# Kernel tuning notes

Hardware: AMD Instinct MI355X
Metric: run time of the kernel (lower is better)

## Reference

```python
import jax, jax.numpy as jnp
import numpy as np

N = 50000; R2 = 200; D = 200; E = 200000; B = 1024
NB = 4; NF = 96; KS = 7; KW = 10; KH = 20
FLAT = (2 * KW - KS + 1) * (KH - KS + 1) * NF  # 18816
EPS = 1e-5


def _bn2d(x, g, b):
    # BatchNorm2d over NCHW with batch statistics
    m = x.mean(axis=(0, 2, 3), keepdims=True)
    v = x.var(axis=(0, 2, 3), keepdims=True)
    return (x - m) * jax.lax.rsqrt(v + EPS) * g[None, :, None, None] + b[None, :, None, None]


def _bn1d(x, g, b):
    m = x.mean(axis=0, keepdims=True)
    v = x.var(axis=0, keepdims=True)
    return (x - m) * jax.lax.rsqrt(v + EPS) * g[None, :] + b[None, :]


def setup_inputs() -> dict:
    key = jax.random.key(0)
    ks = jax.random.split(key, 16)
    s = 0.05
    return {
        'ent_emb': jax.random.normal(ks[0], (N, D)) * s,
        'rel_table': jax.random.normal(ks[1], (R2, D)) * s,
        'basis': jax.random.normal(ks[2], (NB, D, D)) * s,
        'att': jax.random.normal(ks[3], (R2, NB)) * s,
        'root': jax.random.normal(ks[4], (D, D)) * s,
        'gbias': jnp.zeros((D,), jnp.float32),
        'bn0_g': jnp.ones((1,), jnp.float32), 'bn0_b': jnp.zeros((1,), jnp.float32),
        'conv_k': jax.random.normal(ks[5], (NF, 1, KS, KS)) * s,
        'conv_b': jnp.zeros((NF,), jnp.float32),
        'bn1_g': jnp.ones((NF,), jnp.float32), 'bn1_b': jnp.zeros((NF,), jnp.float32),
        'fc_W': jax.random.normal(ks[6], (FLAT, D)) * s,
        'fc_b': jnp.zeros((D,), jnp.float32),
        'bn2_g': jnp.ones((D,), jnp.float32), 'bn2_b': jnp.zeros((D,), jnp.float32),
        'ent_bias': jnp.zeros((N,), jnp.float32),
        'edge_norm': jax.random.uniform(ks[7], (E,)),
        'entity': jnp.arange(N, dtype=jnp.int32),
        'edge_index': jax.random.randint(ks[8], (2, E), 0, N, dtype=jnp.int32),
        'edge_type': jax.random.randint(ks[9], (E,), 0, R2, dtype=jnp.int32),
        'src': jax.random.randint(ks[10], (B,), 0, N, dtype=jnp.int32),
        'rel': jax.random.randint(ks[11], (B,), 0, R2, dtype=jnp.int32),
    }


def reference(ent_emb, rel_table, basis, att, root, gbias, bn0_g, bn0_b,
              conv_k, conv_b, bn1_g, bn1_b, fc_W, fc_b, bn2_g, bn2_b,
              ent_bias, edge_norm, entity, edge_index, edge_type, src, rel):
    # --- MGCNConv: relational message passing ---
    x = ent_emb[entity]                                  # [N, D]
    xj = x[edge_index[0]]                                # gather source nodes [E, D]
    # basis-decomposed per-edge transform: msg_e = x_j @ (att[r_e] . basis)
    xb = jnp.einsum('ei,bio->ebo', xj, basis)            # [E, NB, D]
    msg = jnp.einsum('eb,ebo->eo', att[edge_type], xb)   # [E, D]
    msg = msg * edge_norm[:, None]
    aggr = jax.ops.segment_sum(msg, edge_index[1], num_segments=N)  # scatter-add [N, D]
    h = aggr + x @ root + gbias[None, :]                 # update (root + bias)

    # --- ConvE decoder ---
    src_e = h[src]                                       # [B, D]
    rel_e = rel_table[rel]                               # [B, D]
    stack = jnp.stack([src_e, rel_e], axis=1)            # [B, 2, D]
    xi = jnp.transpose(stack, (0, 2, 1)).reshape(-1, 1, 2 * KW, KH)  # [B,1,20,20]
    xi = _bn2d(xi, bn0_g, bn0_b)
    xi = jax.lax.conv_general_dilated(
        xi, conv_k, (1, 1), 'VALID',
        dimension_numbers=('NCHW', 'OIHW', 'NCHW')) + conv_b[None, :, None, None]
    xi = jax.nn.relu(_bn2d(xi, bn1_g, bn1_b))
    xi = xi.reshape(xi.shape[0], -1) @ fc_W + fc_b       # [B, D]
    xi = jax.nn.relu(_bn1d(xi, bn2_g, bn2_b))
    logits = xi @ h.T + ent_bias[None, :]                # [B, N]
    return jax.nn.sigmoid(logits)
```

## Files before the change

kernel.cpp:

```cpp
#include <hip/hip_runtime.h>
#include <hip/hip_bf16.h>

constexpr int N_ENT = 50000;
constexpr int D     = 200;
constexpr int NE    = 200000;
constexpr int BATCH = 1024;
constexpr int NF    = 96;
constexpr int FLAT  = 18816;
constexpr int KP    = 224;
constexpr float EPS = 1e-5f;

#define DEV static __device__ __forceinline__

typedef __attribute__((ext_vector_type(8))) __bf16 bf16x8;
typedef __attribute__((ext_vector_type(4))) float  f32x4;

DEV float bf2f(unsigned short u){ return __uint_as_float(((unsigned)u) << 16); }
DEV unsigned short f2bf(float f){
    unsigned u = __float_as_uint(f);
    return (unsigned short)((u + 0x7FFF + ((u >> 16) & 1)) >> 16);
}
DEV float sigmoidf(float x){ return 1.f / (1.f + __expf(-x)); }
DEV bf16x8 bzero8(){ bf16x8 v; 
    #pragma unroll
    for (int i = 0; i < 8; ++i) v[i] = (__bf16)0.f; 
    return v; }

__global__ __launch_bounds__(256) void k_pack_wb(const float* __restrict__ basis,
                                                 const float* __restrict__ root,
                                                 unsigned short* __restrict__ wb){
    int idx = blockIdx.x * 256 + threadIdx.x;
    if (idx >= 1008 * KP) return;
    int col = idx / KP, k = idx % KP;
    float v = 0.f;
    if (k < 200){
        if (col < 800){ int o = col >> 2, b = col & 3; v = basis[b * (D*D) + k * D + o]; }
        else if (col < 1000) v = root[k * D + (col - 800)];
    }
    wb[idx] = f2bf(v);
}

__global__ __launch_bounds__(256) void k_prep_eb(const float* __restrict__ ent_emb,
                                                 const int* __restrict__ entity,
                                                 unsigned short* __restrict__ eb){
    int gid = blockIdx.x * 256 + threadIdx.x;
    int m = gid / 28, k0 = (gid % 28) * 8;
    if (m >= 50048) return;
    unsigned short o[8];
    if (m < N_ENT){
        long base = (long)entity[m] * D;
        #pragma unroll
        for (int j = 0; j < 8; ++j){
            int k = k0 + j;
            o[j] = (k < D) ? f2bf(ent_emb[base + k]) : 0;
        }
    } else {
        #pragma unroll
        for (int j = 0; j < 8; ++j) o[j] = 0;
    }
    *(ushort4*)(eb + (long)m * KP + k0)     = make_ushort4(o[0], o[1], o[2], o[3]);
    *(ushort4*)(eb + (long)m * KP + k0 + 4) = make_ushort4(o[4], o[5], o[6], o[7]);
}

__global__ __launch_bounds__(256) void k_gemm_zh_mfma(const unsigned short* __restrict__ eb,
                                                      const unsigned short* __restrict__ wb,
                                                      const float* __restrict__ gbias,
                                                      unsigned short* __restrict__ z,
                                                      float* __restrict__ h){
    const int tid = threadIdx.x, w = tid >> 6, l = tid & 63;
    const int wm = w >> 1, wn = w & 1;
    const int m0 = blockIdx.y * 64 + wm * 32;
    const int n0 = blockIdx.x * 128 + wn * 64;
    const int lr = l & 15, lk = (l >> 4) * 8;
    f32x4 acc[2][4];
    #pragma unroll
    for (int mi = 0; mi < 2; ++mi)
        #pragma unroll
        for (int nj = 0; nj < 4; ++nj) acc[mi][nj] = (f32x4){0.f, 0.f, 0.f, 0.f};
    for (int k0 = 0; k0 < KP; k0 += 32){
        bf16x8 a[2], b[4];
        #pragma unroll
        for (int mi = 0; mi < 2; ++mi)
            a[mi] = *(const bf16x8*)(eb + (long)(m0 + mi*16 + lr) * KP + k0 + lk);
        #pragma unroll
        for (int nj = 0; nj < 4; ++nj){
            int col = n0 + nj*16 + lr;
            b[nj] = (col < 1008) ? *(const bf16x8*)(wb + (long)col * KP + k0 + lk) : bzero8();
        }
        #pragma unroll
        for (int mi = 0; mi < 2; ++mi)
            #pragma unroll
            for (int nj = 0; nj < 4; ++nj)
                acc[mi][nj] = __builtin_amdgcn_mfma_f32_16x16x32_bf16(a[mi], b[nj], acc[mi][nj], 0, 0, 0);
    }
    #pragma unroll
    for (int mi = 0; mi < 2; ++mi)
        #pragma unroll
        for (int r = 0; r < 4; ++r){
            int row = m0 + mi*16 + (l >> 4) * 4 + r;
            if (row >= N_ENT) continue;
            #pragma unroll
            for (int nj = 0; nj < 4; ++nj){
                int col = n0 + nj*16 + lr;
                float v = acc[mi][nj][r];
                if (col < 800)       z[(long)row * 800 + col] = f2bf(v);
                else if (col < 1000) h[row * D + (col - 800)] = v + gbias[col - 800];
            }
        }
}

__global__ __launch_bounds__(256) void k_edge(const unsigned short* __restrict__ z,
                                              float* __restrict__ h,
                                              const int* __restrict__ edge_index,
                                              const int* __restrict__ edge_type,
                                              const float* __restrict__ edge_norm,
                                              const float* __restrict__ att){
    int gtid = blockIdx.x * 256 + threadIdx.x;
    int wave = gtid >> 6, lane = gtid & 63;
    int nw = (gridDim.x * 256) >> 6;
    for (int e = wave; e < NE; e += nw){
        int src = edge_index[e];
        int dst = edge_index[NE + e];
        int r = edge_type[e];
        float nrm = edge_norm[e];
        float w0 = att[r*4+0]*nrm, w1 = att[r*4+1]*nrm, w2 = att[r*4+2]*nrm, w3 = att[r*4+3]*nrm;
        #pragma unroll
        for (int s = 0; s < 4; ++s){
            int d = lane + s * 64;
            if (d < D){
                ushort4 u = *(const ushort4*)(z + ((long)src * D + d) * 4);
                float v = w0*bf2f(u.x) + w1*bf2f(u.y) + w2*bf2f(u.z) + w3*bf2f(u.w);
                atomicAdd(h + dst * D + d, v);
            }
        }
    }
}

DEV void block_reduce2(float& s, float& ss, float* red){
    #pragma unroll
    for (int o = 32; o > 0; o >>= 1){ s += __shfl_down(s, o); ss += __shfl_down(ss, o); }
    int w = threadIdx.x >> 6;
    if ((threadIdx.x & 63) == 0){ red[w*2] = s; red[w*2+1] = ss; }
    __syncthreads();
    if (threadIdx.x == 0){
        #pragma unroll
        for (int i = 1; i < 4; ++i){ s += red[i*2]; ss += red[i*2+1]; }
    }
}

__global__ __launch_bounds__(256) void k_bn0_stats(const float* __restrict__ h,
                                                   const float* __restrict__ rel_table,
                                                   const int* __restrict__ srcb,
                                                   const int* __restrict__ relb,
                                                   float* __restrict__ stats){
    __shared__ float red[8];
    int b = blockIdx.x;
    int sb = srcb[b], rb = relb[b];
    float s = 0.f, ss = 0.f;
    for (int idx = threadIdx.x; idx < 2*D; idx += 256){
        float v = (idx < D) ? h[sb*D + idx] : rel_table[rb*D + (idx - D)];
        s += v; ss += v * v;
    }
    block_reduce2(s, ss, red);
    if (threadIdx.x == 0){ atomicAdd(&stats[0], s); atomicAdd(&stats[1], ss); }
}

__global__ __launch_bounds__(256) void k_h2bf(const float* __restrict__ h,
                                              unsigned short* __restrict__ hb){
    int gid = blockIdx.x * 256 + threadIdx.x;
    int m = gid / 28, k0 = (gid % 28) * 8;
    if (m >= 50048) return;
    unsigned short o[8];
    #pragma unroll
    for (int j = 0; j < 8; ++j){
        int k = k0 + j;
        o[j] = (m < N_ENT && k < D) ? f2bf(h[m*D + k]) : 0;
    }
    *(ushort4*)(hb + (long)m*KP + k0)     = make_ushort4(o[0], o[1], o[2], o[3]);
    *(ushort4*)(hb + (long)m*KP + k0 + 4) = make_ushort4(o[4], o[5], o[6], o[7]);
}

__global__ __launch_bounds__(256) void k_pack_fcw(const float* __restrict__ fc_W,
                                                  unsigned short* __restrict__ fcwt){
    __shared__ float t[32][33];
    int k0 = blockIdx.x * 32, n0 = blockIdx.y * 32;
    int tx = threadIdx.x & 31, ty = threadIdx.x >> 5;
    #pragma unroll
    for (int i = 0; i < 4; ++i){
        int k = k0 + ty + i*8, n = n0 + tx;
        t[ty + i*8][tx] = (n < D) ? fc_W[(long)k * D + n] : 0.f;
    }
    __syncthreads();
    #pragma unroll
    for (int i = 0; i < 4; ++i){
        int n = n0 + ty + i*8, k = k0 + tx;
        if (n < 208) fcwt[(long)n * FLAT + k] = f2bf(t[tx][ty + i*8]);
    }
}

__global__ __launch_bounds__(256) void k_conv(const float* __restrict__ h,
                                              const float* __restrict__ rel_table,
                                              const int* __restrict__ srcb,
                                              const int* __restrict__ relb,
                                              const float* __restrict__ stats,
                                              const float* __restrict__ bn0_g,
                                              const float* __restrict__ bn0_b,
                                              const float* __restrict__ conv_k,
                                              const float* __restrict__ conv_b,
                                              unsigned short* __restrict__ conv_out){
    __shared__ float img[20][20];
    __shared__ float kf[NF * 49];
    int b = blockIdx.x;
    float m0 = stats[0] * (1.f / 409600.f);
    float v0 = stats[1] * (1.f / 409600.f) - m0 * m0;
    float sc = rsqrtf(v0 + EPS) * bn0_g[0];
    float sh = bn0_b[0] - m0 * sc;
    int sb = srcb[b], rb = relb[b];
    for (int idx = threadIdx.x; idx < 400; idx += 256){
        int d = idx >> 1, c = idx & 1;
        float v = c ? rel_table[rb*D + d] : h[sb*D + d];
        img[idx / 20][idx % 20] = v * sc + sh;
    }
    for (int idx = threadIdx.x; idx < NF*49; idx += 256) kf[idx] = conv_k[idx];
    __syncthreads();
    for (int o = threadIdx.x; o < NF*196; o += 256){
        int f = o / 196, p = o % 196, oy = p / 14, ox = p % 14;
        float acc = conv_b[f];
        #pragma unroll
        for (int ky = 0; ky < 7; ++ky)
            #pragma unroll
            for (int kx = 0; kx < 7; ++kx)
                acc += img[oy + ky][ox + kx] * kf[f*49 + ky*7 + kx];
        conv_out[(long)b * FLAT + o] = f2bf(acc);
    }
}

__global__ __launch_bounds__(256) void k_bn1_partial(const unsigned short* __restrict__ conv_out,
                                                     float* __restrict__ s1sum,
                                                     float* __restrict__ s1ss){
    __shared__ float red[8];
    int c = blockIdx.x, b0 = blockIdx.y * 64;
    float s = 0.f, ss = 0.f;
    for (int idx = threadIdx.x; idx < 64*196; idx += 256){
        int b = b0 + idx / 196, p = idx % 196;
        float v = bf2f(conv_out[(long)b * FLAT + c*196 + p]);
        s += v; ss += v * v;
    }
    block_reduce2(s, ss, red);
    if (threadIdx.x == 0){ atomicAdd(&s1sum[c], s); atomicAdd(&s1ss[c], ss); }
}

__global__ __launch_bounds__(128) void k_bn1_final(const float* __restrict__ s1sum,
                                                   const float* __restrict__ s1ss,
                                                   const float* __restrict__ bn1_g,
                                                   const float* __restrict__ bn1_b,
                                                   float* __restrict__ scale1,
                                                   float* __restrict__ shift1){
    int c = threadIdx.x;
    if (c < NF){
        float m = s1sum[c] * (1.f / 200704.f);
        float var = s1ss[c] * (1.f / 200704.f) - m * m;
        float scv = rsqrtf(var + EPS) * bn1_g[c];
        scale1[c] = scv;
        shift1[c] = bn1_b[c] - m * scv;
    }
}

__global__ __launch_bounds__(256) void k_prep_fcA(unsigned short* __restrict__ conv_out,
                                                  const float* __restrict__ scale1,
                                                  const float* __restrict__ shift1){
    int gid = blockIdx.x * 256 + threadIdx.x;
    if (gid >= BATCH * 2352) return;
    long base = (long)gid * 8;
    int k0 = (int)(base % FLAT);
    ushort4 u0 = *(ushort4*)(conv_out + base);
    ushort4 u1 = *(ushort4*)(conv_out + base + 4);
    unsigned short o[8]; unsigned short in[8] = {u0.x,u0.y,u0.z,u0.w,u1.x,u1.y,u1.z,u1.w};
    #pragma unroll
    for (int j = 0; j < 8; ++j){
        int c = (k0 + j) / 196;
        float v = bf2f(in[j]) * scale1[c] + shift1[c];
        o[j] = f2bf(fmaxf(v, 0.f));
    }
    *(ushort4*)(conv_out + base)     = make_ushort4(o[0], o[1], o[2], o[3]);
    *(ushort4*)(conv_out + base + 4) = make_ushort4(o[4], o[5], o[6], o[7]);
}

__global__ __launch_bounds__(256) void k_fc_mfma(const unsigned short* __restrict__ ab,
                                                 const unsigned short* __restrict__ fcwt,
                                                 float* __restrict__ fc_out){
    const int tid = threadIdx.x, w = tid >> 6, l = tid & 63;
    const int wm = w >> 1, wn = w & 1;
    const int m0 = blockIdx.y * 64 + wm * 32;
    const int n0 = blockIdx.x * 64 + wn * 32;
    const int kb = blockIdx.z * 1568;
    const int lr = l & 15, lk = (l >> 4) * 8;
    f32x4 acc[2][2];
    #pragma unroll
    for (int mi = 0; mi < 2; ++mi)
        #pragma unroll
        for (int nj = 0; nj < 2; ++nj) acc[mi][nj] = (f32x4){0.f, 0.f, 0.f, 0.f};
    for (int k0 = kb; k0 < kb + 1568; k0 += 32){
        bf16x8 a[2], b[2];
        #pragma unroll
        for (int mi = 0; mi < 2; ++mi)
            a[mi] = *(const bf16x8*)(ab + (long)(m0 + mi*16 + lr) * FLAT + k0 + lk);
        #pragma unroll
        for (int nj = 0; nj < 2; ++nj){
            int col = n0 + nj*16 + lr;
            b[nj] = (col < 208) ? *(const bf16x8*)(fcwt + (long)col * FLAT + k0 + lk) : bzero8();
        }
        #pragma unroll
        for (int mi = 0; mi < 2; ++mi)
            #pragma unroll
            for (int nj = 0; nj < 2; ++nj)
                acc[mi][nj] = __builtin_amdgcn_mfma_f32_16x16x32_bf16(a[mi], b[nj], acc[mi][nj], 0, 0, 0);
    }
    #pragma unroll
    for (int mi = 0; mi < 2; ++mi)
        #pragma unroll
        for (int r = 0; r < 4; ++r){
            int row = m0 + mi*16 + (l >> 4) * 4 + r;
            #pragma unroll
            for (int nj = 0; nj < 2; ++nj){
                int col = n0 + nj*16 + lr;
                if (col < 208) atomicAdd(&fc_out[row * 208 + col], acc[mi][nj][r]);
            }
        }
}

__global__ __launch_bounds__(256) void k_bn2_stats(const float* __restrict__ fc_out,
                                                   const float* __restrict__ bn2_g,
                                                   const float* __restrict__ bn2_b,
                                                   float* __restrict__ sc2,
                                                   float* __restrict__ sh2){
    __shared__ float red[8];
    int n = blockIdx.x;
    float s = 0.f, ss = 0.f;
    for (int b = threadIdx.x; b < BATCH; b += 256){
        float v = fc_out[b * 208 + n];
        s += v; ss += v * v;
    }
    block_reduce2(s, ss, red);
    if (threadIdx.x == 0){
        float m = s * (1.f / 1024.f);
        float var = ss * (1.f / 1024.f) - m * m;
        float scv = rsqrtf(var + EPS) * bn2_g[n];
        sc2[n] = scv;
        sh2[n] = bn2_b[n] - m * scv;
    }
}

__global__ __launch_bounds__(256) void k_prep_logitsA(const float* __restrict__ fc_out,
                                                      const float* __restrict__ sc2,
                                                      const float* __restrict__ sh2,
                                                      unsigned short* __restrict__ ab_l){
    int idx = blockIdx.x * 256 + threadIdx.x;
    if (idx >= BATCH * KP) return;
    int b = idx / KP, k = idx % KP;
    float v = 0.f;
    if (k < D) v = fmaxf(fc_out[b * 208 + k] * sc2[k] + sh2[k], 0.f);
    ab_l[idx] = f2bf(v);
}

__global__ __launch_bounds__(256) void k_logits_mfma(const unsigned short* __restrict__ ab_l,
                                                     const unsigned short* __restrict__ hb,
                                                     const float* __restrict__ ent_bias,
                                                     float* __restrict__ out){
    const int tid = threadIdx.x, w = tid >> 6, l = tid & 63;
    const int wm = w >> 1, wn = w & 1;
    const int m0 = blockIdx.y * 64 + wm * 32;
    const int n0 = blockIdx.x * 128 + wn * 64;
    const int lr = l & 15, lk = (l >> 4) * 8;
    f32x4 acc[2][4];
    #pragma unroll
    for (int mi = 0; mi < 2; ++mi)
        #pragma unroll
        for (int nj = 0; nj < 4; ++nj) acc[mi][nj] = (f32x4){0.f, 0.f, 0.f, 0.f};
    for (int k0 = 0; k0 < KP; k0 += 32){
        bf16x8 a[2], b[4];
        #pragma unroll
        for (int mi = 0; mi < 2; ++mi)
            a[mi] = *(const bf16x8*)(ab_l + (long)(m0 + mi*16 + lr) * KP + k0 + lk);
        #pragma unroll
        for (int nj = 0; nj < 4; ++nj){
            int cb = n0 + nj*16;
            b[nj] = (cb < N_ENT) ? *(const bf16x8*)(hb + (long)(cb + lr) * KP + k0 + lk) : bzero8();
        }
        #pragma unroll
        for (int mi = 0; mi < 2; ++mi)
            #pragma unroll
            for (int nj = 0; nj < 4; ++nj)
                acc[mi][nj] = __builtin_amdgcn_mfma_f32_16x16x32_bf16(a[mi], b[nj], acc[mi][nj], 0, 0, 0);
    }
    #pragma unroll
    for (int mi = 0; mi < 2; ++mi)
        #pragma unroll
        for (int r = 0; r < 4; ++r){
            int row = m0 + mi*16 + (l >> 4) * 4 + r;
            #pragma unroll
            for (int nj = 0; nj < 4; ++nj){
                int cb = n0 + nj*16;
                if (cb < N_ENT){
                    int col = cb + lr;
                    out[(long)row * N_ENT + col] = sigmoidf(acc[mi][nj][r] + ent_bias[col]);
                }
            }
        }
}

extern "C" void kernel_launch(void* const* d_in, const int* in_sizes, int n_in,
                              void* d_out, int out_size, void* d_ws, size_t ws_size,
                              hipStream_t stream){
    const float* ent_emb   = (const float*)d_in[0];
    const float* rel_table = (const float*)d_in[1];
    const float* basis     = (const float*)d_in[2];
    const float* att       = (const float*)d_in[3];
    const float* root      = (const float*)d_in[4];
    const float* gbias     = (const float*)d_in[5];
    const float* bn0_g     = (const float*)d_in[6];
    const float* bn0_b     = (const float*)d_in[7];
    const float* conv_k    = (const float*)d_in[8];
    const float* conv_b    = (const float*)d_in[9];
    const float* bn1_g     = (const float*)d_in[10];
    const float* bn1_b     = (const float*)d_in[11];
    const float* fc_W      = (const float*)d_in[12];
    const float* bn2_g     = (const float*)d_in[14];
    const float* bn2_b     = (const float*)d_in[15];
    const float* ent_bias  = (const float*)d_in[16];
    const float* edge_norm = (const float*)d_in[17];
    const int*   entity    = (const int*)d_in[18];
    const int*   edge_index= (const int*)d_in[19];
    const int*   edge_type = (const int*)d_in[20];
    const int*   srcb      = (const int*)d_in[21];
    const int*   relb      = (const int*)d_in[22];
    float* out = (float*)d_out;

    char* ws = (char*)d_ws;
    unsigned short* z        = (unsigned short*)(ws);
    unsigned short* hb       = (unsigned short*)(ws);
    unsigned short* fcwt     = (unsigned short*)(ws + 48000000);
    float*          h        = (float*)(ws + 80000000);
    unsigned short* conv_out = (unsigned short*)(ws + 120000000);
    unsigned short* eb       = (unsigned short*)(ws + 120000000);
    unsigned short* wb       = (unsigned short*)(ws + 158535168);
    float*          fc_out   = (float*)(ws + 158986752);
    unsigned short* ab_l     = (unsigned short*)(ws + 159838720);
    float*          stats    = (float*)(ws + 160297472);
    float* s1sum  = stats + 8;
    float* s1ss   = stats + 104;
    float* scale1 = stats + 200;
    float* shift1 = stats + 296;
    float* sc2    = stats + 392;
    float* sh2    = stats + 592;

    hipMemsetAsync(stats, 0, 4096, stream);
    hipMemsetAsync(fc_out, 0, BATCH * 208 * sizeof(float), stream);

    k_pack_wb      <<<(1008 * KP + 255) / 256, 256, 0, stream>>>(basis, root, wb);
    k_prep_eb      <<<(50048 * 28 + 255) / 256, 256, 0, stream>>>(ent_emb, entity, eb);
    k_gemm_zh_mfma <<<dim3(8, 782), 256, 0, stream>>>(eb, wb, gbias, z, h);
    k_edge         <<<2048, 256, 0, stream>>>(z, h, edge_index, edge_type, edge_norm, att);
    k_bn0_stats    <<<BATCH, 256, 0, stream>>>(h, rel_table, srcb, relb, stats);
    k_h2bf         <<<(50048 * 28 + 255) / 256, 256, 0, stream>>>(h, hb);
    k_pack_fcw     <<<dim3(588, 7), 256, 0, stream>>>(fc_W, fcwt);
    k_conv         <<<BATCH, 256, 0, stream>>>(h, rel_table, srcb, relb, stats, bn0_g, bn0_b,
                                               conv_k, conv_b, conv_out);
    k_bn1_partial  <<<dim3(NF, 16), 256, 0, stream>>>(conv_out, s1sum, s1ss);
    k_bn1_final    <<<1, 128, 0, stream>>>(s1sum, s1ss, bn1_g, bn1_b, scale1, shift1);
    k_prep_fcA     <<<(BATCH * 2352 + 255) / 256, 256, 0, stream>>>(conv_out, scale1, shift1);
    k_fc_mfma      <<<dim3(4, 16, 12), 256, 0, stream>>>(conv_out, fcwt, fc_out);
    k_bn2_stats    <<<D, 256, 0, stream>>>(fc_out, bn2_g, bn2_b, sc2, sh2);
    k_prep_logitsA <<<(BATCH * KP + 255) / 256, 256, 0, stream>>>(fc_out, sc2, sh2, ab_l);
    k_logits_mfma  <<<dim3(391, 16), 256, 0, stream>>>(ab_l, hb, ent_bias, out);
}
```

Baseline: 985.2 us.

## Recast ConvE convolution as im2col GEMM on MFMA with pixel-major layout

Replaces the scalar direct 7x7 convolution with an im2col kernel that builds a bf16 [B*196, 64] patch matrix (bias folded in as a ones column) and an MFMA GEMM against packed filters. Conv output becomes pixel-major [B*196, 96], so BN1 stats are recomputed with vectorised row reads, and a new per-batch kernel applies BN1+ReLU and transposes through LDS back to the channel-major layout the FC GEMM expects. This moves the conv arithmetic onto matrix units at the cost of an extra im2col buffer write/read, extra kernel launches, and bf16 rounding of the conv inputs and weights.

```diff
diff --git a/kernel.cpp b/kernel.cpp
--- a/kernel.cpp
+++ b/kernel.cpp
@@ -198,18 +198,25 @@
     }
 }
 
-__global__ __launch_bounds__(256) void k_conv(const float* __restrict__ h,
-                                              const float* __restrict__ rel_table,
-                                              const int* __restrict__ srcb,
-                                              const int* __restrict__ relb,
-                                              const float* __restrict__ stats,
-                                              const float* __restrict__ bn0_g,
-                                              const float* __restrict__ bn0_b,
-                                              const float* __restrict__ conv_k,
-                                              const float* __restrict__ conv_b,
-                                              unsigned short* __restrict__ conv_out){
-    __shared__ float img[20][20];
-    __shared__ float kf[NF * 49];
+__global__ __launch_bounds__(256) void k_pack_ckb(const float* __restrict__ conv_k,
+                                                  const float* __restrict__ conv_b,
+                                                  unsigned short* __restrict__ ckb){
+    for (int idx = threadIdx.x; idx < NF * 64; idx += 256){
+        int f = idx >> 6, k = idx & 63;
+        float v = (k < 49) ? conv_k[f * 49 + k] : (k == 49 ? conv_b[f] : 0.f);
+        ckb[idx] = f2bf(v);
+    }
+}
+
+__global__ __launch_bounds__(256) void k_im2col(const float* __restrict__ h,
+                                               const float* __restrict__ rel_table,
+                                               const int* __restrict__ srcb,
+                                               const int* __restrict__ relb,
+                                               const float* __restrict__ stats,
+                                               const float* __restrict__ bn0_g,
+                                               const float* __restrict__ bn0_b,
+                                               unsigned short* __restrict__ A){
+    __shared__ float img[20][21];
     int b = blockIdx.x;
     float m0 = stats[0] * (1.f / 409600.f);
     float v0 = stats[1] * (1.f / 409600.f) - m0 * m0;
@@ -221,33 +228,91 @@
         float v = c ? rel_table[rb*D + d] : h[sb*D + d];
         img[idx / 20][idx % 20] = v * sc + sh;
     }
-    for (int idx = threadIdx.x; idx < NF*49; idx += 256) kf[idx] = conv_k[idx];
     __syncthreads();
-    for (int o = threadIdx.x; o < NF*196; o += 256){
-        int f = o / 196, p = o % 196, oy = p / 14, ox = p % 14;
-        float acc = conv_b[f];
-        #pragma unroll
-        for (int ky = 0; ky < 7; ++ky)
-            #pragma unroll
-            for (int kx = 0; kx < 7; ++kx)
-                acc += img[oy + ky][ox + kx] * kf[f*49 + ky*7 + kx];
-        conv_out[(long)b * FLAT + o] = f2bf(acc);
-    }
-}
-
-__global__ __launch_bounds__(256) void k_bn1_partial(const unsigned short* __restrict__ conv_out,
-                                                     float* __restrict__ s1sum,
-                                                     float* __restrict__ s1ss){
-    __shared__ float red[8];
-    int c = blockIdx.x, b0 = blockIdx.y * 64;
-    float s = 0.f, ss = 0.f;
-    for (int idx = threadIdx.x; idx < 64*196; idx += 256){
-        int b = b0 + idx / 196, p = idx % 196;
-        float v = bf2f(conv_out[(long)b * FLAT + c*196 + p]);
-        s += v; ss += v * v;
-    }
-    block_reduce2(s, ss, red);
-    if (threadIdx.x == 0){ atomicAdd(&s1sum[c], s); atomicAdd(&s1ss[c], ss); }
+    for (int idx = threadIdx.x; idx < 196 * 8; idx += 256){
+        int p = idx >> 3, g = idx & 7;
+        int oy = p / 14, ox = p % 14, k0 = g * 8;
+        unsigned short o[8];
+        #pragma unroll
+        for (int j = 0; j < 8; ++j){
+            int k = k0 + j;
+            float v = 0.f;
+            if (k < 49){ int ky = k / 7, kx = k % 7; v = img[oy + ky][ox + kx]; }
+            else if (k == 49) v = 1.f;
+            o[j] = f2bf(v);
+        }
+        long base = ((long)b * 196 + p) * 64 + k0;
+        *(ushort4*)(A + base)     = make_ushort4(o[0], o[1], o[2], o[3]);
+        *(ushort4*)(A + base + 4) = make_ushort4(o[4], o[5], o[6], o[7]);
+    }
+}
+
+__global__ __launch_bounds__(256) void k_conv_mfma(const unsigned short* __restrict__ A,
+                                                   const unsigned short* __restrict__ ckb,
+                                                   unsigned short* __restrict__ conv_out){
+    const int tid = threadIdx.x, w = tid >> 6, l = tid & 63;
+    const int m0 = blockIdx.x * 128 + w * 32;
+    const int lr = l & 15, lk = (l >> 4) * 8;
+    f32x4 acc[2][6];
+    #pragma unroll
+    for (int mi = 0; mi < 2; ++mi)
+        #pragma unroll
+        for (int nj = 0; nj < 6; ++nj) acc[mi][nj] = (f32x4){0.f, 0.f, 0.f, 0.f};
+    #pragma unroll
+    for (int k0 = 0; k0 < 64; k0 += 32){
+        bf16x8 a[2], b[6];
+        #pragma unroll
+        for (int mi = 0; mi < 2; ++mi)
+            a[mi] = *(const bf16x8*)(A + (long)(m0 + mi*16 + lr) * 64 + k0 + lk);
+        #pragma unroll
+        for (int nj = 0; nj < 6; ++nj)
+            b[nj] = *(const bf16x8*)(ckb + (nj*16 + lr) * 64 + k0 + lk);
+        #pragma unroll
+        for (int mi = 0; mi < 2; ++mi)
+            #pragma unroll
+            for (int nj = 0; nj < 6; ++nj)
+                acc[mi][nj] = __builtin_amdgcn_mfma_f32_16x16x32_bf16(a[mi], b[nj], acc[mi][nj], 0, 0, 0);
+    }
+    #pragma unroll
+    for (int mi = 0; mi < 2; ++mi)
+        #pragma unroll
+        for (int r = 0; r < 4; ++r){
+            long row = m0 + mi*16 + (l >> 4) * 4 + r;
+            #pragma unroll
+            for (int nj = 0; nj < 6; ++nj)
+                conv_out[row * 96 + nj*16 + lr] = f2bf(acc[mi][nj][r]);
+        }
+}
+
+__global__ __launch_bounds__(256) void k_bn1_stats2(const unsigned short* __restrict__ conv_out,
+                                                    float* __restrict__ s1sum,
+                                                    float* __restrict__ s1ss){
+    __shared__ float lsum[96], lss[96];
+    int tid = threadIdx.x;
+    if (tid < 96){ lsum[tid] = 0.f; lss[tid] = 0.f; }
+    __syncthreads();
+    if (tid < 192){
+        int fg = tid % 24, rs = tid / 24;
+        long r0 = (long)blockIdx.x * 784;
+        float s[4] = {}, ss[4] = {};
+        for (int i = 0; i < 98; ++i){
+            long r = r0 + rs + i * 8;
+            ushort4 u = *(const ushort4*)(conv_out + r * 96 + fg * 4);
+            float v0 = bf2f(u.x), v1 = bf2f(u.y), v2 = bf2f(u.z), v3 = bf2f(u.w);
+            s[0] += v0; ss[0] += v0*v0; s[1] += v1; ss[1] += v1*v1;
+            s[2] += v2; ss[2] += v2*v2; s[3] += v3; ss[3] += v3*v3;
+        }
+        #pragma unroll
+        for (int j = 0; j < 4; ++j){
+            atomicAdd(&lsum[fg*4 + j], s[j]);
+            atomicAdd(&lss[fg*4 + j], ss[j]);
+        }
+    }
+    __syncthreads();
+    if (tid < 96){
+        atomicAdd(&s1sum[tid], lsum[tid]);
+        atomicAdd(&s1ss[tid], lss[tid]);
+    }
 }
 
 __global__ __launch_bounds__(128) void k_bn1_final(const float* __restrict__ s1sum,
@@ -266,24 +331,36 @@
     }
 }
 
-__global__ __launch_bounds__(256) void k_prep_fcA(unsigned short* __restrict__ conv_out,
-                                                  const float* __restrict__ scale1,
-                                                  const float* __restrict__ shift1){
-    int gid = blockIdx.x * 256 + threadIdx.x;
-    if (gid >= BATCH * 2352) return;
-    long base = (long)gid * 8;
-    int k0 = (int)(base % FLAT);
-    ushort4 u0 = *(ushort4*)(conv_out + base);
-    ushort4 u1 = *(ushort4*)(conv_out + base + 4);
-    unsigned short o[8]; unsigned short in[8] = {u0.x,u0.y,u0.z,u0.w,u1.x,u1.y,u1.z,u1.w};
-    #pragma unroll
-    for (int j = 0; j < 8; ++j){
-        int c = (k0 + j) / 196;
-        float v = bf2f(in[j]) * scale1[c] + shift1[c];
-        o[j] = f2bf(fmaxf(v, 0.f));
-    }
-    *(ushort4*)(conv_out + base)     = make_ushort4(o[0], o[1], o[2], o[3]);
-    *(ushort4*)(conv_out + base + 4) = make_ushort4(o[4], o[5], o[6], o[7]);
+__global__ __launch_bounds__(256) void k_bn1_tr(const unsigned short* __restrict__ conv_out,
+                                                const float* __restrict__ scale1,
+                                                const float* __restrict__ shift1,
+                                                unsigned short* __restrict__ fcA){
+    __shared__ unsigned short lds[FLAT];
+    int b = blockIdx.x, tid = threadIdx.x;
+    for (int idx = tid; idx < 2352; idx += 256){
+        long base = (long)b * FLAT + idx * 8;
+        ushort4 u0 = *(const ushort4*)(conv_out + base);
+        ushort4 u1 = *(const ushort4*)(conv_out + base + 4);
+        unsigned short in[8] = {u0.x,u0.y,u0.z,u0.w,u1.x,u1.y,u1.z,u1.w};
+        unsigned short o[8];
+        int f0 = (idx * 8) % 96;
+        #pragma unroll
+        for (int j = 0; j < 8; ++j){
+            float v = bf2f(in[j]) * scale1[f0 + j] + shift1[f0 + j];
+            o[j] = f2bf(fmaxf(v, 0.f));
+        }
+        *(ushort4*)(lds + idx*8)     = make_ushort4(o[0], o[1], o[2], o[3]);
+        *(ushort4*)(lds + idx*8 + 4) = make_ushort4(o[4], o[5], o[6], o[7]);
+    }
+    __syncthreads();
+    for (int idx = tid; idx < 4704; idx += 256){
+        int q = idx * 4;
+        int f = q / 196, p0 = q % 196;
+        unsigned short o[4];
+        #pragma unroll
+        for (int j = 0; j < 4; ++j) o[j] = lds[(p0 + j) * 96 + f];
+        *(ushort4*)(fcA + (long)b * FLAT + q) = make_ushort4(o[0], o[1], o[2], o[3]);
+    }
 }
 
 __global__ __launch_bounds__(256) void k_fc_mfma(const unsigned short* __restrict__ ab,
@@ -439,7 +516,10 @@
     char* ws = (char*)d_ws;
     unsigned short* z        = (unsigned short*)(ws);
     unsigned short* hb       = (unsigned short*)(ws);
-    unsigned short* fcwt     = (unsigned short*)(ws + 48000000);
+    unsigned short* ckb      = (unsigned short*)(ws + 22500096);
+    unsigned short* imA      = (unsigned short*)(ws + 24000000);
+    unsigned short* fcA      = (unsigned short*)(ws + 24000000);
+    unsigned short* fcwt     = (unsigned short*)(ws + 63000000);
     float*          h        = (float*)(ws + 80000000);
     unsigned short* conv_out = (unsigned short*)(ws + 120000000);
     unsigned short* eb       = (unsigned short*)(ws + 120000000);
@@ -464,12 +544,14 @@
     k_bn0_stats    <<<BATCH, 256, 0, stream>>>(h, rel_table, srcb, relb, stats);
     k_h2bf         <<<(50048 * 28 + 255) / 256, 256, 0, stream>>>(h, hb);
     k_pack_fcw     <<<dim3(588, 7), 256, 0, stream>>>(fc_W, fcwt);
-    k_conv         <<<BATCH, 256, 0, stream>>>(h, rel_table, srcb, relb, stats, bn0_g, bn0_b,
-                                               conv_k, conv_b, conv_out);
-    k_bn1_partial  <<<dim3(NF, 16), 256, 0, stream>>>(conv_out, s1sum, s1ss);
+    k_pack_ckb     <<<1, 256, 0, stream>>>(conv_k, conv_b, ckb);
+    k_im2col       <<<BATCH, 256, 0, stream>>>(h, rel_table, srcb, relb, stats,
+                                               bn0_g, bn0_b, imA);
+    k_conv_mfma    <<<1568, 256, 0, stream>>>(imA, ckb, conv_out);
+    k_bn1_stats2   <<<256, 256, 0, stream>>>(conv_out, s1sum, s1ss);
     k_bn1_final    <<<1, 128, 0, stream>>>(s1sum, s1ss, bn1_g, bn1_b, scale1, shift1);
-    k_prep_fcA     <<<(BATCH * 2352 + 255) / 256, 256, 0, stream>>>(conv_out, scale1, shift1);
-    k_fc_mfma      <<<dim3(4, 16, 12), 256, 0, stream>>>(conv_out, fcwt, fc_out);
+    k_bn1_tr       <<<BATCH, 256, 0, stream>>>(conv_out, scale1, shift1, fcA);
+    k_fc_mfma      <<<dim3(4, 16, 12), 256, 0, stream>>>(fcA, fcwt, fc_out);
     k_bn2_stats    <<<D, 256, 0, stream>>>(fc_out, bn2_g, bn2_b, sc2, sh2);
     k_prep_logitsA <<<(BATCH * KP + 255) / 256, 256, 0, stream>>>(fc_out, sc2, sh2, ab_l);
     k_logits_mfma  <<<dim3(391, 16), 256, 0, stream>>>(ab_l, hb, ent_bias, out);
```

Result: faster. 893.8 us (-9.3%).
